# Kernel optimization log

Measured on AMD Instinct MI355X. Metric: run time of the kernel, lower is better.

The kernel has to match this reference:

```python
import jax, jax.numpy as jnp
import numpy as np

RCR = 5.2
RCA = 3.5
ETA_R = np.array([16.0], np.float32)                      # (1,)
SHF_R = (0.9 + 0.26875 * np.arange(16)).astype(np.float32)  # (16,)
ETA_A = np.array([8.0], np.float32)                       # (1,)
ZETA = np.array([32.0], np.float32)                       # (1,)
SHF_A = np.array([0.9, 1.55, 2.2, 2.85], np.float32)      # (4,)
SHF_Z = (np.pi / 16 + (np.pi / 8) * np.arange(8)).astype(np.float32)  # (8,)
NUM_SPECIES = 4
C, A = 16, 64
EPS = 1e-8  # torch cosine_similarity eps

# unordered species-pair index table: (s1, s2) -> triu pair id (10 pairs for 4 species)
_tbl = np.zeros((NUM_SPECIES, NUM_SPECIES), np.int32)
_k = 0
for _a in range(NUM_SPECIES):
    for _b in range(_a, NUM_SPECIES):
        _tbl[_a, _b] = _k
        _tbl[_b, _a] = _k
        _k += 1
PAIR_TABLE = jnp.asarray(_tbl)
NUM_SP_PAIRS = _k  # 10

IDX_I, IDX_J = np.triu_indices(A, k=1)  # neighbor pair combinations, P = A*(A-1)/2


def _cutoff_cosine(d, rc):
    return jnp.where(d <= rc, 0.5 * jnp.cos(np.pi * d / rc) + 0.5, 0.0)


def setup_inputs() -> dict:
    key = jax.random.key(0)
    k1, k2 = jax.random.split(key)
    species = jax.random.randint(k1, (C, A), 0, NUM_SPECIES)
    # spread atoms over a realistic box so distances span the cutoffs
    coordinates = jax.random.normal(k2, (C, A, 3), dtype=jnp.float32) * 4.0
    return {"species": species, "coordinates": coordinates}


def reference(species, coordinates):
    f32 = coordinates.dtype
    # vec[c,i,j,:] = R_i - R_j  (matches coordinates.unsqueeze(2)-unsqueeze(1))
    vec = coordinates[:, :, None, :] - coordinates[:, None, :, :]  # (C,A,A,3)
    i_idx = jnp.arange(A)
    # valid neighbor: not self, not padding (species == -1)
    valid = (i_idx[:, None] != i_idx[None, :])[None] & (species[:, None, :] != -1)  # (C,A,A)
    vec_safe = jnp.where(valid[..., None], vec, 1.0)
    d = jnp.linalg.norm(vec_safe, axis=-1)          # (C,A,A)
    d = jnp.where(valid, d, RCR + 1.0)

    # ---- radial subAEV terms: 0.25 * exp(-EtaR (d - ShfR)^2) * fc ----
    fc = _cutoff_cosine(d, RCR)                      # (C,A,A)
    shf_r = jnp.asarray(SHF_R)
    eta_r = jnp.asarray(ETA_R)[0]
    rt = 0.25 * jnp.exp(-eta_r * (d[..., None] - shf_r) ** 2) * fc[..., None]  # (C,A,A,16)
    rt = rt * valid[..., None].astype(f32)
    onehot_s = (species[:, :, None] == jnp.arange(NUM_SPECIES)).astype(f32)  # (C,A,S)
    radial_aev = jnp.einsum('cijr,cjs->cisr', rt, onehot_s)  # (C,A,S,16)
    radial_aev = radial_aev.reshape(C, A, NUM_SPECIES * SHF_R.size)

    # ---- angular subAEV terms over neighbor pairs ----
    v1 = vec[:, :, IDX_I, :]                         # (C,A,P,3)
    v2 = vec[:, :, IDX_J, :]
    pair_valid = valid[:, :, IDX_I] & valid[:, :, IDX_J]  # (C,A,P)
    v1s = jnp.where(pair_valid[..., None], v1, 1.0)
    v2s = jnp.where(pair_valid[..., None], v2, 1.0)
    d1 = jnp.linalg.norm(v1s, axis=-1)
    d2 = jnp.linalg.norm(v2s, axis=-1)
    d1 = jnp.where(pair_valid, d1, RCA + 1.0)
    d2 = jnp.where(pair_valid, d2, RCA + 1.0)
    cos_ang = 0.95 * jnp.sum(v1s * v2s, -1) / (jnp.maximum(d1, EPS) * jnp.maximum(d2, EPS))
    angles = jnp.arccos(cos_ang)                     # |cos|<=0.95 so safe
    fcj1 = _cutoff_cosine(d1, RCA)
    fcj2 = _cutoff_cosine(d2, RCA)
    # broadcast layout (..., EtaA=1, Zeta=1, ShfA=4, ShfZ=8) -> flatten to 32
    shf_a = jnp.asarray(SHF_A).reshape(1, 1, 4, 1)
    shf_z = jnp.asarray(SHF_Z).reshape(1, 1, 1, 8)
    zeta = jnp.asarray(ZETA)[0]
    eta_a = jnp.asarray(ETA_A)[0]
    ang = angles[..., None, None, None, None]        # (C,A,P,1,1,1,1)
    dm = ((d1 + d2) / 2)[..., None, None, None, None]
    factor1 = ((1 + jnp.cos(ang - shf_z)) / 2) ** zeta
    factor2 = jnp.exp(-eta_a * (dm - shf_a) ** 2)
    at = 2 * factor1 * factor2 * fcj1[..., None, None, None, None] * fcj2[..., None, None, None, None]
    P = IDX_I.size
    at = at.reshape(C, A, P, 32) * pair_valid[..., None].astype(f32)  # (C,A,P,32)

    # species-pair one-hot over the P neighbor pairs
    sp1 = jnp.clip(species[:, IDX_I], 0, NUM_SPECIES - 1)  # (C,P); padding masked by pair_valid
    sp2 = jnp.clip(species[:, IDX_J], 0, NUM_SPECIES - 1)
    pid = PAIR_TABLE[sp1, sp2]                       # (C,P)
    onehot_p = (pid[..., None] == jnp.arange(NUM_SP_PAIRS)).astype(f32)  # (C,P,10)
    angular_aev = jnp.einsum('cipz,cpt->citz', at, onehot_p)  # (C,A,10,32)
    angular_aev = angular_aev.reshape(C, A, NUM_SP_PAIRS * 32)

    return jnp.concatenate([radial_aev, angular_aev], axis=-1)  # (C,A,384)
```

## Files before the change

### kernel.cpp

```cpp
#include <hip/hip_runtime.h>

#define RCR 5.2f
#define RCA 3.5f
#define PI_F 3.14159265358979323846f

__global__ __launch_bounds__(256)
void aev_kernel(const int* __restrict__ species,
                const float* __restrict__ coords,
                float* __restrict__ out)
{
    const int blk = blockIdx.x;
    const int c   = blk >> 6;
    const int i   = blk & 63;
    const int tid = threadIdx.x;
    const int l   = tid & 63;
    const int w   = tid >> 6;

    const int gbase = (c * 64 + l) * 3;
    float x = coords[gbase + 0];
    float y = coords[gbase + 1];
    float z = coords[gbase + 2];
    int  sp = species[c * 64 + l];

    float xi = __shfl(x, i);
    float yi = __shfl(y, i);
    float zi = __shfl(z, i);

    float rx = xi - x, ry = yi - y, rz = zi - z;
    float d  = sqrtf(rx * rx + ry * ry + rz * rz);
    bool valid  = (l != i) && (sp != -1);
    bool rvalid = valid && (d <= RCR);
    bool avalid = valid && (d <= RCA);

    __shared__ float4 ang0[64];
    __shared__ float4 ang1[64];
    __shared__ float4 radf[64];
    __shared__ int    pairab[1953];
    __shared__ float  acc[320];
    __shared__ float  raccs[64];

    for (int t = tid; t < 320; t += 256) acc[t] = 0.f;
    if (tid < 64) raccs[tid] = 0.f;

    unsigned long long rmask = __ballot(rvalid);
    unsigned long long amask = __ballot(avalid);
    const int nr = __popcll(rmask);
    const int n  = __popcll(amask);

    if (w == 0) {
        const unsigned long long below = (l == 0) ? 0ull : (~0ull >> (64 - l));
        if (rvalid) {
            int pos = __popcll(rmask & below);
            radf[pos] = make_float4(d,
                                    0.5f * __cosf(PI_F * d * (1.0f / RCR)) + 0.5f,
                                    __int_as_float(sp), 0.f);
        }
        if (avalid) {
            int pos = __popcll(amask & below);
            ang0[pos] = make_float4(rx, ry, rz, d);
            ang1[pos] = make_float4(1.0f / fmaxf(d, 1e-8f),
                                    0.5f * __cosf(PI_F * d * (1.0f / RCA)) + 0.5f,
                                    __int_as_float(sp), 0.f);
        }
    }
    if (l < n) {
        const int base = l * (n - 1) - (l * (l - 1)) / 2;
        for (int b = l + 1 + w; b < n; b += 4)
            pairab[base + (b - l - 1)] = (l << 6) | b;
    }
    __syncthreads();

    const int   s   = l >> 4;
    const float shf = 0.9f + 0.26875f * (float)(l & 15);
    float racc = 0.f;
    for (int m = w; m < nr; m += 4) {
        float4 rv  = radf[m];
        float  dd  = rv.x - shf;
        float  term = 0.25f * __expf(-16.f * dd * dd) * rv.y;
        racc += (__float_as_int(rv.z) == s) ? term : 0.f;
    }
    atomicAdd(&raccs[l], racc);

    const int   sub  = l & 31;
    const float shfa = 0.9f + 0.65f * (float)(sub >> 3);
    const float shfz = PI_F / 16.f + (PI_F / 8.f) * (float)(sub & 7);
    const float czv  = __cosf(shfz);
    const float szv  = __sinf(shfz);
    const int   np   = (n * (n - 1)) >> 1;
    const int   half = l >> 5;

    int p0_first = w * 2;
    int p_pf = p0_first + half;
    int ab   = (p_pf < np) ? pairab[p_pf] : 0;
    for (int p0 = p0_first; p0 < np; p0 += 8) {
        const int pc   = p0 + half;
        const int ab_c = ab;
        const int pn   = p0 + 8 + half;
        if (pn < np) ab = pairab[pn];
        if (pc < np) {
            const int a = ab_c >> 6, b = ab_c & 63;
            float4 A0 = ang0[a], A1 = ang1[a];
            float4 B0 = ang0[b], B1 = ang1[b];
            float dot = A0.x * B0.x + A0.y * B0.y + A0.z * B0.z;
            float ca  = 0.95f * dot * A1.x * B1.x;
            float sa  = sqrtf(fmaxf(0.f, 1.f - ca * ca));
            float dm  = 0.5f * (A0.w + B0.w);
            float fprod = 2.f * A1.y * B1.y;
            int s1 = __float_as_int(A1.z), s2 = __float_as_int(B1.z);
            int mn = min(s1, s2), mx = max(s1, s2);
            int pid = ((mn * (7 - mn)) >> 1) + mx;
            float cdz = ca * czv + sa * szv;
            float t = 0.5f + 0.5f * cdz;
            t = t * t; t = t * t; t = t * t; t = t * t; t = t * t;
            float u = dm - shfa;
            float val = t * __expf(-8.f * u * u) * fprod;
            atomicAdd(&acc[pid * 32 + sub], val);
        }
    }
    __syncthreads();

    const long ob = (long)blk * 384;
    if (tid < 64) out[ob + tid] = raccs[tid];
    for (int t = tid; t < 320; t += 256) out[ob + 64 + t] = acc[t];
}

extern "C" void kernel_launch(void* const* d_in, const int* in_sizes, int n_in,
                              void* d_out, int out_size, void* d_ws, size_t ws_size,
                              hipStream_t stream) {
    const int* species  = (const int*)d_in[0];
    const float* coords = (const float*)d_in[1];
    float* out          = (float*)d_out;
    aev_kernel<<<dim3(16 * 64), dim3(256), 0, stream>>>(species, coords, out);
}
```

Before: 62.49 us.

## Compute neighbor pair indices analytically and drop shared pair table

Removes the shared-memory pair index table and its construction pass, and instead decodes each linear pair index into (a,b) with a triangular-number inverse via sqrt and correction steps. The radial accumulation switches from shared atomics to per-wave partial buffers that are summed at output time. The angular loop is unrolled by two pairs per iteration. This cuts LDS footprint and the table-building work at the cost of extra ALU per pair.

```diff
diff --git a/kernel.cpp b/kernel.cpp
--- a/kernel.cpp
+++ b/kernel.cpp
@@ -35,12 +35,10 @@
     __shared__ float4 ang0[64];
     __shared__ float4 ang1[64];
     __shared__ float4 radf[64];
-    __shared__ int    pairab[1953];
     __shared__ float  acc[320];
-    __shared__ float  raccs[64];
+    __shared__ float  raccs4[4][64];
 
     for (int t = tid; t < 320; t += 256) acc[t] = 0.f;
-    if (tid < 64) raccs[tid] = 0.f;
 
     unsigned long long rmask = __ballot(rvalid);
     unsigned long long amask = __ballot(avalid);
@@ -63,11 +61,6 @@
                                     __int_as_float(sp), 0.f);
         }
     }
-    if (l < n) {
-        const int base = l * (n - 1) - (l * (l - 1)) / 2;
-        for (int b = l + 1 + w; b < n; b += 4)
-            pairab[base + (b - l - 1)] = (l << 6) | b;
-    }
     __syncthreads();
 
     const int   s   = l >> 4;
@@ -79,7 +72,7 @@
         float  term = 0.25f * __expf(-16.f * dd * dd) * rv.y;
         racc += (__float_as_int(rv.z) == s) ? term : 0.f;
     }
-    atomicAdd(&raccs[l], racc);
+    raccs4[w][l] = racc;
 
     const int   sub  = l & 31;
     const float shfa = 0.9f + 0.65f * (float)(sub >> 3);
@@ -87,18 +80,18 @@
     const float czv  = __cosf(shfz);
     const float szv  = __sinf(shfz);
     const int   np   = (n * (n - 1)) >> 1;
-    const int   half = l >> 5;
+    const int   lane_pair = (w << 1) + (l >> 5);
 
-    int p0_first = w * 2;
-    int p_pf = p0_first + half;
-    int ab   = (p_pf < np) ? pairab[p_pf] : 0;
-    for (int p0 = p0_first; p0 < np; p0 += 8) {
-        const int pc   = p0 + half;
-        const int ab_c = ab;
-        const int pn   = p0 + 8 + half;
-        if (pn < np) ab = pairab[pn];
-        if (pc < np) {
-            const int a = ab_c >> 6, b = ab_c & 63;
+    auto do_pair = [&](int p) {
+        if (p < np) {
+            int rev = np - 1 - p;
+            int k = (int)floorf((sqrtf((float)(8 * rev + 1)) - 1.0f) * 0.5f);
+            int tk = (k * (k + 1)) >> 1;
+            if (tk > rev)                          { --k; tk = (k * (k + 1)) >> 1; }
+            else if (((k + 1) * (k + 2)) >> 1 <= rev) { ++k; tk = (k * (k + 1)) >> 1; }
+            const int a = n - 2 - k;
+            const int b = n - 1 - (rev - tk);
+
             float4 A0 = ang0[a], A1 = ang1[a];
             float4 B0 = ang0[b], B1 = ang1[b];
             float dot = A0.x * B0.x + A0.y * B0.y + A0.z * B0.z;
@@ -116,11 +109,18 @@
             float val = t * __expf(-8.f * u * u) * fprod;
             atomicAdd(&acc[pid * 32 + sub], val);
         }
+    };
+
+    for (int p0 = 0; p0 < np; p0 += 16) {
+        do_pair(p0 + lane_pair);
+        do_pair(p0 + 8 + lane_pair);
     }
     __syncthreads();
 
     const long ob = (long)blk * 384;
-    if (tid < 64) out[ob + tid] = raccs[tid];
+    if (tid < 64)
+        out[ob + tid] = raccs4[0][tid] + raccs4[1][tid]
+                      + raccs4[2][tid] + raccs4[3][tid];
     for (int t = tid; t < 320; t += 256) out[ob + 64 + t] = acc[t];
 }
 
```

New measurement: 60.57 us. 3.1% less time.
